# Kernel tuning notes

Hardware: AMD Instinct MI355X
Metric: run time of the kernel (lower is better)

Reference implementation:

```python
import jax, jax.numpy as jnp
import numpy as np

N_NODES = 50000
N_EDGES = 250000
EMBED_DIM = 256
LEAKY_SLOPE = 0.01
LN_EPS = 1e-5


def setup_inputs() -> dict:
    key = jax.random.key(0)
    ks = jax.random.split(key, 6)
    d = EMBED_DIM
    H = jax.random.normal(ks[0], (N_NODES, d), dtype=jnp.float32)
    E = jax.random.normal(ks[1], (N_EDGES, d), dtype=jnp.float32)
    ht = jax.random.randint(ks[2], (N_EDGES, 2), 0, N_NODES, dtype=jnp.int32)
    # Linear(4d -> d) weights, torch layout [out, in], scaled like kaiming-uniform-ish
    scale = 1.0 / np.sqrt(4 * d)
    W_fwd = jax.random.normal(ks[3], (d, 4 * d), dtype=jnp.float32) * scale
    W_back = jax.random.normal(ks[4], (d, 4 * d), dtype=jnp.float32) * scale
    b_fwd = jnp.zeros((d,), dtype=jnp.float32)
    b_back = jnp.zeros((d,), dtype=jnp.float32)
    gamma = jnp.ones((d,), dtype=jnp.float32)
    beta = jnp.zeros((d,), dtype=jnp.float32)
    return {"H": H, "E": E, "ht": ht, "W_fwd": W_fwd, "b_fwd": b_fwd,
            "W_back": W_back, "b_back": b_back, "gamma": gamma, "beta": beta}


def _calc_messages(H, E, idx, W, b):
    Hh = H[idx]                                   # [m, d]
    raw = jnp.concatenate([Hh, E, Hh + E, Hh * E], axis=1)  # [m, 4d]
    return raw @ W.T + b                          # [m, d]


def reference(H, E, ht, W_fwd, b_fwd, W_back, b_back, gamma, beta):
    n = H.shape[0]
    heads = ht[:, 0]
    tails = ht[:, 1]
    messages_fwd = _calc_messages(H, E, heads, W_fwd, b_fwd)
    messages_back = _calc_messages(H, E, tails, W_back, b_back)
    # forward messages go to tails, backward messages go to heads
    msg_dst = jnp.concatenate([tails, heads])     # [2m]
    messages = jnp.concatenate([messages_fwd, messages_back], axis=0)  # [2m, d]
    agg = jax.ops.segment_sum(messages, msg_dst, num_segments=n)       # [n, d]
    cnt = jax.ops.segment_sum(jnp.ones((messages.shape[0],), dtype=messages.dtype),
                              msg_dst, num_segments=n)                 # [n]
    agg = agg / jnp.maximum(cnt, 1.0)[:, None]    # scatter-mean; empty nodes stay 0
    x = jax.nn.leaky_relu(agg, LEAKY_SLOPE) + H
    mu = jnp.mean(x, axis=-1, keepdims=True)
    var = jnp.var(x, axis=-1, keepdims=True)
    out = (x - mu) * jax.lax.rsqrt(var + LN_EPS) * gamma + beta
    return out
```

## Files before the change

kernel.cpp:

```cpp
#include <hip/hip_runtime.h>
#include <hip/hip_bf16.h>

#define D 256
#define NB 128
#define BK 64
#define NCK 24
#define NPB 64
#define LEAKY 0.01f
#define EPS 1e-5f

typedef float f32x4 __attribute__((ext_vector_type(4)));
typedef short s16x8 __attribute__((ext_vector_type(8)));

#define GLL16(g, l) __builtin_amdgcn_global_load_lds(                      \
    (const __attribute__((address_space(1))) unsigned int*)(g),            \
    (__attribute__((address_space(3))) unsigned int*)(l), 16, 0, 0)

__device__ __forceinline__ unsigned short f2bf(float f){
  union { float f; unsigned int u; } v; v.f = f;
  unsigned int u = v.u;
  return (unsigned short)((u + 0x7fffu + ((u >> 16) & 1u)) >> 16);
}

__global__ void prep_w(const float* __restrict__ Wf, const float* __restrict__ Wb,
                       unsigned short* __restrict__ Wimg)
{
  int i = blockIdx.x * 256 + threadIdx.x;
  int inner = i & 8191;
  int t = i >> 13;
  int c = t % 24;
  int h = t / 24;
  int j = inner >> 6, k = inner & 63;
  int kg  = c * 64 + k;
  int dir = kg / 768;
  int kl  = kg - dir * 768;
  int part = kl >> 8, x = kl & 255;
  const float* row = (dir ? Wb : Wf) + (long)(h * NB + j) * (4 * D);
  float v;
  if (part == 0)      v = row[256 + x] + row[512 + x];
  else if (part == 1) v = row[768 + x];
  else                v = row[x] + row[512 + x];
  int boff = (j * 128 + k * 2) ^ ((j & 7) << 4);
  *(unsigned short*)((char*)Wimg + (size_t)t * 16384 + boff) = f2bf(v);
}

__global__ void count2(const int* __restrict__ ht, int* __restrict__ cnt,
                       int n_edges, int n_nodes)
{
  int e = blockIdx.x * 256 + threadIdx.x;
  if (e < n_edges){
    atomicAdd(&cnt[ht[2*e+1]], 1);
    atomicAdd(&cnt[n_nodes + ht[2*e]], 1);
  }
}

__global__ void scan_sums(const int* __restrict__ cnt, int* __restrict__ bsum, int N2)
{
  int t = threadIdx.x, b = blockIdx.x;
  int i = b * 1024 + t;
  int v = (i < N2) ? cnt[i] : 0;
  #pragma unroll
  for (int o = 32; o > 0; o >>= 1) v += __shfl_down(v, o);
  __shared__ int red[16];
  int lane = t & 63, wv = t >> 6;
  if (lane == 0) red[wv] = v;
  __syncthreads();
  if (t == 0){ int s = 0; for (int k = 0; k < 16; ++k) s += red[k]; bsum[b] = s; }
}

__global__ void scan_bases(const int* __restrict__ bsum, int* __restrict__ bases, int nb)
{
  if (threadIdx.x == 0 && blockIdx.x == 0){
    int a = 0;
    for (int k = 0; k < nb; ++k){ bases[k] = a; a += bsum[k]; }
  }
}

__global__ void scan_off(const int* __restrict__ cnt, const int* __restrict__ bases,
                         int* __restrict__ off, int N2)
{
  int t = threadIdx.x, b = blockIdx.x;
  int i = b * 1024 + t;
  int v = (i < N2) ? cnt[i] : 0;
  int lane = t & 63, wv = t >> 6;
  int x = v;
  #pragma unroll
  for (int o = 1; o < 64; o <<= 1){ int y = __shfl_up(x, o); if (lane >= o) x += y; }
  __shared__ int ws[16];
  if (lane == 63) ws[wv] = x;
  __syncthreads();
  if (t == 0){ int a = 0; for (int k = 0; k < 16; ++k){ int tmp = ws[k]; ws[k] = a; a += tmp; } }
  __syncthreads();
  if (i < N2) off[i] = bases[b] + ws[wv] + x - v;
}

__global__ void scatter_msgs(const int* __restrict__ ht, const int* __restrict__ off,
                             int* __restrict__ cursor, int* __restrict__ perm,
                             int* __restrict__ hS, int n_edges, int n_nodes)
{
  int m = blockIdx.x * 256 + threadIdx.x;
  if (m >= 2 * n_edges) return;
  int e  = (m < n_edges) ? m : m - n_edges;
  int hd = ht[2*e], tl = ht[2*e+1];
  int dst = (m < n_edges) ? tl : hd;
  int oth = (m < n_edges) ? hd : tl;
  int idx = ((m < n_edges) ? 0 : n_nodes) + dst;
  int pos = off[idx] + atomicAdd(&cursor[idx], 1);
  perm[pos] = e; hS[pos] = oth;
}

__global__ __launch_bounds__(256, 8) void aggregate(
    const float* __restrict__ H, const float* __restrict__ E,
    const int* __restrict__ perm, const int* __restrict__ hS,
    const int* __restrict__ off, const int* __restrict__ cnt_i,
    unsigned short* __restrict__ S, int n_edges, int n_nodes)
{
  const int t   = threadIdx.x;
  const int dir = blockIdx.x & 1;
  const int b   = blockIdx.x >> 1;
  const int n0  = b * NPB;

  for (int i = 0; i < NPB; ++i){
    int n = n0 + i;
    if (n >= n_nodes) break;
    int idx  = dir * n_nodes + n;
    int base = off[idx];
    int cn   = cnt_i[idx];
    float s0 = 0.f, s1 = 0.f, s2 = 0.f;
    int k = 0;
    for (; k + 1 < cn; k += 2){
      int p0 = base + k, p1 = p0 + 1;
      int e0 = perm[p0], h0 = hS[p0];
      int e1 = perm[p1], h1 = hS[p1];
      float ev0 = E[(size_t)e0 * D + t];
      float hv0 = H[(size_t)h0 * D + t];
      float ev1 = E[(size_t)e1 * D + t];
      float hv1 = H[(size_t)h1 * D + t];
      s0 += ev0 + ev1;
      s1 += ev0 * hv0 + ev1 * hv1;
      s2 += hv0 + hv1;
    }
    if (k < cn){
      int p0 = base + k;
      int e0 = perm[p0], h0 = hS[p0];
      float ev0 = E[(size_t)e0 * D + t];
      float hv0 = H[(size_t)h0 * D + t];
      s0 += ev0; s1 += ev0 * hv0; s2 += hv0;
    }
    size_t o = (size_t)n * 1536 + dir * 768 + t;
    S[o]       = f2bf(s0);
    S[o + 256] = f2bf(s1);
    S[o + 512] = f2bf(s2);
  }
}

__global__ __launch_bounds__(512, 4) void node_gemm(
    const unsigned short* __restrict__ S, const unsigned short* __restrict__ Wimg,
    float* __restrict__ agg, int n_nodes)
{
  __shared__ char smem[65536];
  char (*sAl)[16384] = (char(*)[16384])smem;
  char (*sBl)[16384] = (char(*)[16384])(smem + 32768);

  const int bid = blockIdx.x;
  const int h   = bid & 1;
  const int n0  = (bid >> 1) * 128;

  const int tid  = threadIdx.x;
  const int lane = tid & 63;
  const int wave = tid >> 6;

  const char* wq = (const char*)Wimg + (size_t)h * NCK * 16384;
  const char* Sb = (const char*)S;

  f32x4 acc[4][2];
  #pragma unroll
  for (int mi = 0; mi < 4; ++mi)
    #pragma unroll
    for (int ni = 0; ni < 2; ++ni)
      acc[mi][ni] = (f32x4){0.f, 0.f, 0.f, 0.f};

  const int rlo = lane & 15;
  const int khi = lane >> 4;
  const int wm = wave >> 2;
  const int wn = wave & 3;

  const int arow = wave * 8 + (lane >> 3);
  const int aunit = ((lane & 7) ^ (lane >> 3)) * 16;
  const size_t an0 = (size_t)((n0 + arow      < n_nodes) ? n0 + arow      : n_nodes - 1);
  const size_t an1 = (size_t)((n0 + 64 + arow < n_nodes) ? n0 + 64 + arow : n_nodes - 1);

  #define STAGE_A(c, buf) {                                                  \
    const char* s0 = Sb + an0 * 3072 + (size_t)(c) * 128 + aunit;            \
    const char* s1 = Sb + an1 * 3072 + (size_t)(c) * 128 + aunit;            \
    char* d = &sAl[buf][wave * 1024];                                        \
    GLL16(s0, d);                                                            \
    GLL16(s1, d + 8192);                                                     \
  }

  #define STAGE_B(c, buf) {                                                  \
    const char* srcb = wq + (size_t)(c) * 16384 + wave * 2048 + lane * 16;   \
    char* db = &sBl[buf][wave * 2048];                                       \
    GLL16(srcb,        db);                                                  \
    GLL16(srcb + 1024, db + 1024);                                           \
  }

  STAGE_A(0, 0);
  STAGE_B(0, 0);
  __syncthreads();

  #pragma unroll
  for (int c = 0; c < NCK; ++c){
    const int cur = c & 1;
    if (c + 1 < NCK){
      STAGE_A(c + 1, cur ^ 1);
      STAGE_B(c + 1, cur ^ 1);
    }
    #pragma unroll
    for (int ks = 0; ks < 2; ++ks){
      const int kb = (ks * 32 + khi * 8) * 2;
      s16x8 af[4], bfr[2];
      #pragma unroll
      for (int mi = 0; mi < 4; ++mi){
        int row = wm * 64 + mi * 16 + rlo;
        af[mi] = *(const s16x8*)(&sAl[cur][(row * 128 + kb) ^ ((row & 7) << 4)]);
      }
      #pragma unroll
      for (int ni = 0; ni < 2; ++ni){
        int col = wn * 32 + ni * 16 + rlo;
        bfr[ni] = *(const s16x8*)(&sBl[cur][(col * 128 + kb) ^ ((col & 7) << 4)]);
      }
      #pragma unroll
      for (int mi = 0; mi < 4; ++mi)
        #pragma unroll
        for (int ni = 0; ni < 2; ++ni)
          acc[mi][ni] = __builtin_amdgcn_mfma_f32_16x16x32_bf16(
              af[mi], bfr[ni], acc[mi][ni], 0, 0, 0);
    }
    if (c + 1 < NCK) __syncthreads();
  }
  #undef STAGE_A
  #undef STAGE_B

  #pragma unroll
  for (int ni = 0; ni < 2; ++ni){
    const int col = h * NB + wn * 32 + ni * 16 + rlo;
    #pragma unroll
    for (int mi = 0; mi < 4; ++mi){
      #pragma unroll
      for (int r = 0; r < 4; ++r){
        int n = n0 + wm * 64 + mi * 16 + khi * 4 + r;
        if (n < n_nodes)
          agg[(size_t)n * D + col] = acc[mi][ni][r];
      }
    }
  }
}

__global__ __launch_bounds__(256) void finish(
    const float* __restrict__ agg, const int* __restrict__ cnt_i,
    const float* __restrict__ H, const float* __restrict__ bias_f,
    const float* __restrict__ bias_b, const float* __restrict__ gamma,
    const float* __restrict__ beta, float* __restrict__ out, int n_nodes)
{
  const int n = blockIdx.x;
  const int j = threadIdx.x;
  int cf = cnt_i[n], cb = cnt_i[n_nodes + n];
  float c = (float)(cf + cb); c = c < 1.f ? 1.f : c;
  float a = (agg[(size_t)n * D + j] + (float)cf * bias_f[j] + (float)cb * bias_b[j]) / c;
  float x = (a > 0.f ? a : LEAKY * a) + H[(size_t)n * D + j];
  float s1 = x, s2 = x * x;
  #pragma unroll
  for (int off = 32; off > 0; off >>= 1){
    s1 += __shfl_xor(s1, off);
    s2 += __shfl_xor(s2, off);
  }
  __shared__ float rs[8];
  if ((j & 63) == 0){ rs[j >> 6] = s1; rs[4 + (j >> 6)] = s2; }
  __syncthreads();
  float t1 = rs[0] + rs[1] + rs[2] + rs[3];
  float t2 = rs[4] + rs[5] + rs[6] + rs[7];
  float mu = t1 * (1.f / D);
  float var = t2 * (1.f / D) - mu * mu;
  float r = rsqrtf(var + EPS);
  out[(size_t)n * D + j] = (x - mu) * r * gamma[j] + beta[j];
}

extern "C" void kernel_launch(void* const* d_in, const int* in_sizes, int n_in,
                              void* d_out, int out_size, void* d_ws, size_t ws_size,
                              hipStream_t stream)
{
  const float* H      = (const float*)d_in[0];
  const float* E      = (const float*)d_in[1];
  const int*   ht     = (const int*)d_in[2];
  const float* W_fwd  = (const float*)d_in[3];
  const float* b_fwd  = (const float*)d_in[4];
  const float* W_back = (const float*)d_in[5];
  const float* b_back = (const float*)d_in[6];
  const float* gamma  = (const float*)d_in[7];
  const float* beta   = (const float*)d_in[8];
  float* out = (float*)d_out;

  const int n_nodes = in_sizes[0] / D;
  const int n_edges = in_sizes[2] / 2;
  const int N2 = 2 * n_nodes;
  const int NM = 2 * n_edges;

  char* p = (char*)d_ws;
  float* agg    = (float*)p;  p += (size_t)n_nodes * D * 4;
  int*   cnt_i  = (int*)p;    p += (size_t)N2 * 4;
  int*   cursor = (int*)p;    p += (size_t)N2 * 4;
  int*   off    = (int*)p;    p += (size_t)N2 * 4;
  int*   bsum   = (int*)p;    p += 128 * 4;
  int*   bases  = (int*)p;    p += 128 * 4;
  int*   perm   = (int*)p;    p += (size_t)NM * 4;
  int*   hS     = (int*)p;    p += (size_t)NM * 4;
  unsigned short* S = (unsigned short*)p; p += (size_t)n_nodes * 1536 * 2;
  p = (char*)(((size_t)p + 255) & ~(size_t)255);
  unsigned short* Wimg = (unsigned short*)p;

  const int nscan = (N2 + 1023) / 1024;

  hipMemsetAsync(cnt_i, 0, (size_t)N2 * 2 * 4, stream);
  prep_w<<<(2 * NCK * NB * BK) / 256, 256, 0, stream>>>(W_fwd, W_back, Wimg);
  count2<<<(n_edges + 255) / 256, 256, 0, stream>>>(ht, cnt_i, n_edges, n_nodes);
  scan_sums<<<nscan, 1024, 0, stream>>>(cnt_i, bsum, N2);
  scan_bases<<<1, 64, 0, stream>>>(bsum, bases, nscan);
  scan_off<<<nscan, 1024, 0, stream>>>(cnt_i, bases, off, N2);
  scatter_msgs<<<(NM + 255) / 256, 256, 0, stream>>>(ht, off, cursor, perm, hS,
                                                     n_edges, n_nodes);
  const int nblk = (n_nodes + NPB - 1) / NPB;
  aggregate<<<2 * nblk, 256, 0, stream>>>(H, E, perm, hS, off, cnt_i, S,
                                          n_edges, n_nodes);
  const int nbm = (n_nodes + 127) / 128;
  node_gemm<<<nbm * 2, 512, 0, stream>>>(S, Wimg, agg, n_nodes);
  finish<<<n_nodes, 256, 0, stream>>>(agg, cnt_i, H, b_fwd, b_back, gamma, beta,
                                      out, n_nodes);
}
```

Before: 366.9 us.

## Flatten aggregation over block's message range with segment-boundary flushes

Aggregation no longer loops per node with a dependent off/cnt lookup and a short inner loop. Each block now walks the contiguous range of sorted messages for its node span with 4-way unrolled independent gathers. A per-message destination array written during scatter lets it detect segment boundaries and flush partial sums. Nodes with no messages are zeroed up front. This exposes more memory-level parallelism for low-degree nodes, at the cost of an extra index array write and read and data-dependent branches.

```diff
diff --git a/kernel.cpp b/kernel.cpp
--- a/kernel.cpp
+++ b/kernel.cpp
@@ -96,7 +96,8 @@
 
 __global__ void scatter_msgs(const int* __restrict__ ht, const int* __restrict__ off,
                              int* __restrict__ cursor, int* __restrict__ perm,
-                             int* __restrict__ hS, int n_edges, int n_nodes)
+                             int* __restrict__ hS, int* __restrict__ dstS,
+                             int n_edges, int n_nodes)
 {
   int m = blockIdx.x * 256 + threadIdx.x;
   if (m >= 2 * n_edges) return;
@@ -106,52 +107,72 @@
   int oth = (m < n_edges) ? hd : tl;
   int idx = ((m < n_edges) ? 0 : n_nodes) + dst;
   int pos = off[idx] + atomicAdd(&cursor[idx], 1);
-  perm[pos] = e; hS[pos] = oth;
+  perm[pos] = e; hS[pos] = oth; dstS[pos] = dst;
 }
 
 __global__ __launch_bounds__(256, 8) void aggregate(
     const float* __restrict__ H, const float* __restrict__ E,
     const int* __restrict__ perm, const int* __restrict__ hS,
-    const int* __restrict__ off, const int* __restrict__ cnt_i,
-    unsigned short* __restrict__ S, int n_edges, int n_nodes)
+    const int* __restrict__ dstS, const int* __restrict__ off,
+    const int* __restrict__ cnt_i, unsigned short* __restrict__ S,
+    int n_edges, int n_nodes)
 {
   const int t   = threadIdx.x;
   const int dir = blockIdx.x & 1;
   const int b   = blockIdx.x >> 1;
   const int n0  = b * NPB;
-
-  for (int i = 0; i < NPB; ++i){
-    int n = n0 + i;
-    if (n >= n_nodes) break;
-    int idx  = dir * n_nodes + n;
-    int base = off[idx];
-    int cn   = cnt_i[idx];
-    float s0 = 0.f, s1 = 0.f, s2 = 0.f;
-    int k = 0;
-    for (; k + 1 < cn; k += 2){
-      int p0 = base + k, p1 = p0 + 1;
-      int e0 = perm[p0], h0 = hS[p0];
-      int e1 = perm[p1], h1 = hS[p1];
-      float ev0 = E[(size_t)e0 * D + t];
-      float hv0 = H[(size_t)h0 * D + t];
-      float ev1 = E[(size_t)e1 * D + t];
-      float hv1 = H[(size_t)h1 * D + t];
-      s0 += ev0 + ev1;
-      s1 += ev0 * hv0 + ev1 * hv1;
-      s2 += hv0 + hv1;
+  if (n0 >= n_nodes) return;
+  int nend = n0 + NPB; if (nend > n_nodes) nend = n_nodes;
+
+  for (int n = n0; n < nend; ++n){
+    if (cnt_i[dir * n_nodes + n] == 0){
+      size_t o = (size_t)n * 1536 + dir * 768 + t;
+      S[o] = 0; S[o + 256] = 0; S[o + 512] = 0;
     }
-    if (k < cn){
-      int p0 = base + k;
-      int e0 = perm[p0], h0 = hS[p0];
-      float ev0 = E[(size_t)e0 * D + t];
-      float hv0 = H[(size_t)h0 * D + t];
-      s0 += ev0; s1 += ev0 * hv0; s2 += hv0;
-    }
-    size_t o = (size_t)n * 1536 + dir * 768 + t;
-    S[o]       = f2bf(s0);
-    S[o + 256] = f2bf(s1);
-    S[o + 512] = f2bf(s2);
-  }
+  }
+
+  const int idx0 = dir * n_nodes + n0;
+  const int idxe = dir * n_nodes + nend;
+  const int m0 = off[idx0];
+  const int m1 = (idxe < 2 * n_nodes) ? off[idxe] : 2 * n_edges;
+  if (m0 >= m1) return;
+
+  float s0 = 0.f, s1 = 0.f, s2 = 0.f;
+  int cur = dstS[m0];
+
+  #define FLUSH(d) {                                                        \
+    size_t o = (size_t)(d) * 1536 + dir * 768 + t;                          \
+    S[o] = f2bf(s0); S[o + 256] = f2bf(s1); S[o + 512] = f2bf(s2);          \
+    s0 = 0.f; s1 = 0.f; s2 = 0.f;                                           \
+  }
+
+  int m = m0;
+  for (; m + 4 <= m1; m += 4){
+    int p0 = perm[m],   p1 = perm[m+1], p2 = perm[m+2], p3 = perm[m+3];
+    int q0 = hS[m],     q1 = hS[m+1],   q2 = hS[m+2],   q3 = hS[m+3];
+    int d0 = dstS[m],   d1 = dstS[m+1], d2 = dstS[m+2], d3 = dstS[m+3];
+    float e0 = E[(size_t)p0 * D + t], e1 = E[(size_t)p1 * D + t];
+    float e2 = E[(size_t)p2 * D + t], e3 = E[(size_t)p3 * D + t];
+    float h0 = H[(size_t)q0 * D + t], h1 = H[(size_t)q1 * D + t];
+    float h2 = H[(size_t)q2 * D + t], h3 = H[(size_t)q3 * D + t];
+    if (d0 != cur){ FLUSH(cur); cur = d0; }
+    s0 += e0; s1 += e0 * h0; s2 += h0;
+    if (d1 != cur){ FLUSH(cur); cur = d1; }
+    s0 += e1; s1 += e1 * h1; s2 += h1;
+    if (d2 != cur){ FLUSH(cur); cur = d2; }
+    s0 += e2; s1 += e2 * h2; s2 += h2;
+    if (d3 != cur){ FLUSH(cur); cur = d3; }
+    s0 += e3; s1 += e3 * h3; s2 += h3;
+  }
+  for (; m < m1; ++m){
+    int d = dstS[m];
+    if (d != cur){ FLUSH(cur); cur = d; }
+    float ev = E[(size_t)perm[m] * D + t];
+    float hv = H[(size_t)hS[m] * D + t];
+    s0 += ev; s1 += ev * hv; s2 += hv;
+  }
+  FLUSH(cur);
+  #undef FLUSH
 }
 
 __global__ __launch_bounds__(512, 4) void node_gemm(
@@ -315,6 +336,7 @@
   int*   bases  = (int*)p;    p += 128 * 4;
   int*   perm   = (int*)p;    p += (size_t)NM * 4;
   int*   hS     = (int*)p;    p += (size_t)NM * 4;
+  int*   dstS   = (int*)p;    p += (size_t)NM * 4;
   unsigned short* S = (unsigned short*)p; p += (size_t)n_nodes * 1536 * 2;
   p = (char*)(((size_t)p + 255) & ~(size_t)255);
   unsigned short* Wimg = (unsigned short*)p;
@@ -327,10 +349,10 @@
   scan_sums<<<nscan, 1024, 0, stream>>>(cnt_i, bsum, N2);
   scan_bases<<<1, 64, 0, stream>>>(bsum, bases, nscan);
   scan_off<<<nscan, 1024, 0, stream>>>(cnt_i, bases, off, N2);
-  scatter_msgs<<<(NM + 255) / 256, 256, 0, stream>>>(ht, off, cursor, perm, hS,
+  scatter_msgs<<<(NM + 255) / 256, 256, 0, stream>>>(ht, off, cursor, perm, hS, dstS,
                                                      n_edges, n_nodes);
   const int nblk = (n_nodes + NPB - 1) / NPB;
-  aggregate<<<2 * nblk, 256, 0, stream>>>(H, E, perm, hS, off, cnt_i, S,
+  aggregate<<<2 * nblk, 256, 0, stream>>>(H, E, perm, hS, dstS, off, cnt_i, S,
                                           n_edges, n_nodes);
   const int nbm = (n_nodes + 127) / 128;
   node_gemm<<<nbm * 2, 512, 0, stream>>>(S, Wimg, agg, n_nodes);
```

Result: slower. 421.7 us (+14.9%).

## Stage edge indices in LDS and interleave two nodes per aggregate iteration

Applied to the files above, without the earlier changes.

The aggregate kernel now loads each block's contiguous range of perm and hS indices into shared memory once, falling back to global reads when the range exceeds MCAP. It then processes two nodes per loop iteration (i and i+32) in an interleaved fashion. The intent is to cut dependent global index loads and to raise memory-level parallelism across independent gather chains. The cost is 16KB of LDS per block, which may reduce occupancy, plus divergence when the two nodes have different degrees.

```diff
diff --git a/kernel.cpp b/kernel.cpp
--- a/kernel.cpp
+++ b/kernel.cpp
@@ -6,6 +6,7 @@
 #define BK 64
 #define NCK 24
 #define NPB 64
+#define MCAP 2048
 #define LEAKY 0.01f
 #define EPS 1e-5f
 
@@ -115,42 +116,65 @@
     const int* __restrict__ off, const int* __restrict__ cnt_i,
     unsigned short* __restrict__ S, int n_edges, int n_nodes)
 {
+  __shared__ int sIdx[2][MCAP];
   const int t   = threadIdx.x;
   const int dir = blockIdx.x & 1;
   const int b   = blockIdx.x >> 1;
   const int n0  = b * NPB;
-
-  for (int i = 0; i < NPB; ++i){
-    int n = n0 + i;
-    if (n >= n_nodes) break;
-    int idx  = dir * n_nodes + n;
-    int base = off[idx];
-    int cn   = cnt_i[idx];
-    float s0 = 0.f, s1 = 0.f, s2 = 0.f;
-    int k = 0;
-    for (; k + 1 < cn; k += 2){
-      int p0 = base + k, p1 = p0 + 1;
-      int e0 = perm[p0], h0 = hS[p0];
-      int e1 = perm[p1], h1 = hS[p1];
-      float ev0 = E[(size_t)e0 * D + t];
-      float hv0 = H[(size_t)h0 * D + t];
-      float ev1 = E[(size_t)e1 * D + t];
-      float hv1 = H[(size_t)h1 * D + t];
-      s0 += ev0 + ev1;
-      s1 += ev0 * hv0 + ev1 * hv1;
-      s2 += hv0 + hv1;
-    }
-    if (k < cn){
-      int p0 = base + k;
-      int e0 = perm[p0], h0 = hS[p0];
-      float ev0 = E[(size_t)e0 * D + t];
-      float hv0 = H[(size_t)h0 * D + t];
-      s0 += ev0; s1 += ev0 * hv0; s2 += hv0;
-    }
-    size_t o = (size_t)n * 1536 + dir * 768 + t;
-    S[o]       = f2bf(s0);
-    S[o + 256] = f2bf(s1);
-    S[o + 512] = f2bf(s2);
+  if (n0 >= n_nodes) return;
+  int nend = n0 + NPB; if (nend > n_nodes) nend = n_nodes;
+
+  const int idx0 = dir * n_nodes + n0;
+  const int idxe = dir * n_nodes + nend;
+  const int m0 = off[idx0];
+  const int m1 = (idxe < 2 * n_nodes) ? off[idxe] : 2 * n_edges;
+  const int cnt = m1 - m0;
+  const bool fit = (cnt <= MCAP);
+  if (fit){
+    for (int k = t; k < cnt; k += 256){
+      sIdx[0][k] = perm[m0 + k];
+      sIdx[1][k] = hS[m0 + k];
+    }
+  }
+  __syncthreads();
+
+  const int half = NPB / 2;
+  for (int i = 0; i < half; ++i){
+    int nA = n0 + i;
+    int nB = n0 + half + i;
+    if (nA >= n_nodes) break;
+    bool vB = (nB < nend);
+    int idxA = dir * n_nodes + nA;
+    int baseA = off[idxA] - m0, cnA = cnt_i[idxA];
+    int baseB = 0, cnB = 0;
+    if (vB){ int idxB = dir * n_nodes + nB; baseB = off[idxB] - m0; cnB = cnt_i[idxB]; }
+    float a0 = 0.f, a1 = 0.f, a2 = 0.f;
+    float b0 = 0.f, b1 = 0.f, b2 = 0.f;
+    int kmax = cnA > cnB ? cnA : cnB;
+    for (int k = 0; k < kmax; ++k){
+      if (k < cnA){
+        int p, q;
+        if (fit){ p = sIdx[0][baseA + k]; q = sIdx[1][baseA + k]; }
+        else    { p = perm[m0 + baseA + k]; q = hS[m0 + baseA + k]; }
+        float ev = E[(size_t)p * D + t];
+        float hv = H[(size_t)q * D + t];
+        a0 += ev; a1 += ev * hv; a2 += hv;
+      }
+      if (k < cnB){
+        int p, q;
+        if (fit){ p = sIdx[0][baseB + k]; q = sIdx[1][baseB + k]; }
+        else    { p = perm[m0 + baseB + k]; q = hS[m0 + baseB + k]; }
+        float ev = E[(size_t)p * D + t];
+        float hv = H[(size_t)q * D + t];
+        b0 += ev; b1 += ev * hv; b2 += hv;
+      }
+    }
+    size_t oA = (size_t)nA * 1536 + dir * 768 + t;
+    S[oA] = f2bf(a0); S[oA + 256] = f2bf(a1); S[oA + 512] = f2bf(a2);
+    if (vB){
+      size_t oB = (size_t)nB * 1536 + dir * 768 + t;
+      S[oB] = f2bf(b0); S[oB + 256] = f2bf(b1); S[oB + 512] = f2bf(b2);
+    }
   }
 }
 
```

After: 445.2 us. 1.21x slower.

## Pre-cast E and H to bf16 and restructure aggregate to one wave per node

Applied to the files above, without the earlier changes.

Adds a cast kernel that converts E and H to bf16 up front, so the gather in aggregate reads half the bytes per edge row. Aggregate now assigns each wave its own 16 nodes, with each lane handling 4 contiguous features through 8-byte loads, instead of the whole block walking 64 nodes one scalar per thread. The bf16 buffers share workspace with agg, which is written only later. In exchange the cast adds a full read and write pass over E and H, and inputs are rounded to bf16 before the product, which loses precision.

```diff
diff --git a/kernel.cpp b/kernel.cpp
--- a/kernel.cpp
+++ b/kernel.cpp
@@ -20,6 +20,17 @@
   union { float f; unsigned int u; } v; v.f = f;
   unsigned int u = v.u;
   return (unsigned short)((u + 0x7fffu + ((u >> 16) & 1u)) >> 16);
+}
+__device__ __forceinline__ unsigned int cvtpk(float lo, float hi){
+  unsigned int r;
+  asm("v_cvt_pk_bf16_f32 %0, %1, %2" : "=v"(r) : "v"(lo), "v"(hi));
+  return r;
+}
+__device__ __forceinline__ float bflo(unsigned int u){
+  union { unsigned int u; float f; } v; v.u = u << 16; return v.f;
+}
+__device__ __forceinline__ float bfhi(unsigned int u){
+  union { unsigned int u; float f; } v; v.u = u & 0xffff0000u; return v.f;
 }
 
 __global__ void prep_w(const float* __restrict__ Wf, const float* __restrict__ Wb,
@@ -44,6 +55,19 @@
   *(unsigned short*)((char*)Wimg + (size_t)t * 16384 + boff) = f2bf(v);
 }
 
+__global__ void cast_bf(const float* __restrict__ src,
+                        unsigned short* __restrict__ dst, int n8)
+{
+  int i = blockIdx.x * 256 + threadIdx.x;
+  if (i >= n8) return;
+  const float4* s = (const float4*)src + (size_t)i * 2;
+  float4 a = s[0], b = s[1];
+  uint4 w;
+  w.x = cvtpk(a.x, a.y); w.y = cvtpk(a.z, a.w);
+  w.z = cvtpk(b.x, b.y); w.w = cvtpk(b.z, b.w);
+  ((uint4*)dst)[i] = w;
+}
+
 __global__ void count2(const int* __restrict__ ht, int* __restrict__ cnt,
                        int n_edges, int n_nodes)
 {
@@ -110,47 +134,58 @@
 }
 
 __global__ __launch_bounds__(256, 8) void aggregate(
-    const float* __restrict__ H, const float* __restrict__ E,
+    const unsigned short* __restrict__ Ebf, const unsigned short* __restrict__ Hbf,
     const int* __restrict__ perm, const int* __restrict__ hS,
     const int* __restrict__ off, const int* __restrict__ cnt_i,
     unsigned short* __restrict__ S, int n_edges, int n_nodes)
 {
-  const int t   = threadIdx.x;
+  const int lane = threadIdx.x & 63;
+  const int g    = threadIdx.x >> 6;
+  const int c4   = lane * 4;
   const int dir = blockIdx.x & 1;
   const int b   = blockIdx.x >> 1;
-  const int n0  = b * NPB;
-
-  for (int i = 0; i < NPB; ++i){
+  const int n0  = b * NPB + g * 16;
+
+  for (int i = 0; i < 16; ++i){
     int n = n0 + i;
     if (n >= n_nodes) break;
     int idx  = dir * n_nodes + n;
     int base = off[idx];
     int cn   = cnt_i[idx];
-    float s0 = 0.f, s1 = 0.f, s2 = 0.f;
+    float s0a=0.f,s0b=0.f,s0c=0.f,s0d=0.f;
+    float s1a=0.f,s1b=0.f,s1c=0.f,s1d=0.f;
+    float s2a=0.f,s2b=0.f,s2c=0.f,s2d=0.f;
     int k = 0;
-    for (; k + 1 < cn; k += 2){
-      int p0 = base + k, p1 = p0 + 1;
-      int e0 = perm[p0], h0 = hS[p0];
-      int e1 = perm[p1], h1 = hS[p1];
-      float ev0 = E[(size_t)e0 * D + t];
-      float hv0 = H[(size_t)h0 * D + t];
-      float ev1 = E[(size_t)e1 * D + t];
-      float hv1 = H[(size_t)h1 * D + t];
-      s0 += ev0 + ev1;
-      s1 += ev0 * hv0 + ev1 * hv1;
-      s2 += hv0 + hv1;
-    }
-    if (k < cn){
-      int p0 = base + k;
-      int e0 = perm[p0], h0 = hS[p0];
-      float ev0 = E[(size_t)e0 * D + t];
-      float hv0 = H[(size_t)h0 * D + t];
-      s0 += ev0; s1 += ev0 * hv0; s2 += hv0;
-    }
-    size_t o = (size_t)n * 1536 + dir * 768 + t;
-    S[o]       = f2bf(s0);
-    S[o + 256] = f2bf(s1);
-    S[o + 512] = f2bf(s2);
+    for (; k + 2 <= cn; k += 2){
+      int p0 = perm[base+k], p1 = perm[base+k+1];
+      int q0 = hS[base+k],   q1 = hS[base+k+1];
+      uint2 e0 = *(const uint2*)(Ebf + (size_t)p0 * D + c4);
+      uint2 e1 = *(const uint2*)(Ebf + (size_t)p1 * D + c4);
+      uint2 h0 = *(const uint2*)(Hbf + (size_t)q0 * D + c4);
+      uint2 h1 = *(const uint2*)(Hbf + (size_t)q1 * D + c4);
+      float ea0=bflo(e0.x), eb0=bfhi(e0.x), ec0=bflo(e0.y), ed0=bfhi(e0.y);
+      float ea1=bflo(e1.x), eb1=bfhi(e1.x), ec1=bflo(e1.y), ed1=bfhi(e1.y);
+      float ha0=bflo(h0.x), hb0=bfhi(h0.x), hc0=bflo(h0.y), hd0=bfhi(h0.y);
+      float ha1=bflo(h1.x), hb1=bfhi(h1.x), hc1=bflo(h1.y), hd1=bfhi(h1.y);
+      s0a += ea0 + ea1; s0b += eb0 + eb1; s0c += ec0 + ec1; s0d += ed0 + ed1;
+      s1a += ea0*ha0 + ea1*ha1; s1b += eb0*hb0 + eb1*hb1;
+      s1c += ec0*hc0 + ec1*hc1; s1d += ed0*hd0 + ed1*hd1;
+      s2a += ha0 + ha1; s2b += hb0 + hb1; s2c += hc0 + hc1; s2d += hd0 + hd1;
+    }
+    for (; k < cn; ++k){
+      int p = perm[base+k], q = hS[base+k];
+      uint2 ev = *(const uint2*)(Ebf + (size_t)p * D + c4);
+      uint2 hv = *(const uint2*)(Hbf + (size_t)q * D + c4);
+      float ea=bflo(ev.x), eb=bfhi(ev.x), ec=bflo(ev.y), ed=bfhi(ev.y);
+      float ha=bflo(hv.x), hb=bfhi(hv.x), hc=bflo(hv.y), hd=bfhi(hv.y);
+      s0a += ea; s0b += eb; s0c += ec; s0d += ed;
+      s1a += ea*ha; s1b += eb*hb; s1c += ec*hc; s1d += ed*hd;
+      s2a += ha; s2b += hb; s2c += hc; s2d += hd;
+    }
+    size_t o = (size_t)n * 1536 + dir * 768 + c4;
+    *(uint2*)(S + o)       = (uint2){cvtpk(s0a, s0b), cvtpk(s0c, s0d)};
+    *(uint2*)(S + o + 256) = (uint2){cvtpk(s1a, s1b), cvtpk(s1c, s1d)};
+    *(uint2*)(S + o + 512) = (uint2){cvtpk(s2a, s2b), cvtpk(s2c, s2d)};
   }
 }
 
@@ -307,7 +342,6 @@
   const int NM = 2 * n_edges;
 
   char* p = (char*)d_ws;
-  float* agg    = (float*)p;  p += (size_t)n_nodes * D * 4;
   int*   cnt_i  = (int*)p;    p += (size_t)N2 * 4;
   int*   cursor = (int*)p;    p += (size_t)N2 * 4;
   int*   off    = (int*)p;    p += (size_t)N2 * 4;
@@ -317,12 +351,22 @@
   int*   hS     = (int*)p;    p += (size_t)NM * 4;
   unsigned short* S = (unsigned short*)p; p += (size_t)n_nodes * 1536 * 2;
   p = (char*)(((size_t)p + 255) & ~(size_t)255);
+  char* regionX = p;
+  unsigned short* Ebf = (unsigned short*)regionX;
+  unsigned short* Hbf = (unsigned short*)(regionX + (size_t)n_edges * D * 2);
+  float* agg = (float*)regionX;
+  size_t xbytes = (size_t)n_edges * D * 2 + (size_t)n_nodes * D * 2;
+  size_t abytes = (size_t)n_nodes * D * 4;
+  p = regionX + (xbytes > abytes ? xbytes : abytes);
+  p = (char*)(((size_t)p + 255) & ~(size_t)255);
   unsigned short* Wimg = (unsigned short*)p;
 
   const int nscan = (N2 + 1023) / 1024;
 
   hipMemsetAsync(cnt_i, 0, (size_t)N2 * 2 * 4, stream);
   prep_w<<<(2 * NCK * NB * BK) / 256, 256, 0, stream>>>(W_fwd, W_back, Wimg);
+  cast_bf<<<((n_edges * D / 8) + 255) / 256, 256, 0, stream>>>(E, Ebf, n_edges * D / 8);
+  cast_bf<<<((n_nodes * D / 8) + 255) / 256, 256, 0, stream>>>(H, Hbf, n_nodes * D / 8);
   count2<<<(n_edges + 255) / 256, 256, 0, stream>>>(ht, cnt_i, n_edges, n_nodes);
   scan_sums<<<nscan, 1024, 0, stream>>>(cnt_i, bsum, N2);
   scan_bases<<<1, 64, 0, stream>>>(bsum, bases, nscan);
@@ -330,7 +374,7 @@
   scatter_msgs<<<(NM + 255) / 256, 256, 0, stream>>>(ht, off, cursor, perm, hS,
                                                      n_edges, n_nodes);
   const int nblk = (n_nodes + NPB - 1) / NPB;
-  aggregate<<<2 * nblk, 256, 0, stream>>>(H, E, perm, hS, off, cnt_i, S,
+  aggregate<<<2 * nblk, 256, 0, stream>>>(Ebf, Hbf, perm, hS, off, cnt_i, S,
                                           n_edges, n_nodes);
   const int nbm = (n_nodes + 127) / 128;
   node_gemm<<<nbm * 2, 512, 0, stream>>>(S, Wimg, agg, n_nodes);
```

Measured after the change: 392.0 us. 6.8% more time.
